# Performance work log

Measured on AMD Instinct MI355X. Metric: run time of the kernel, lower is better.

Reference implementation:

```python
import jax, jax.numpy as jnp
import numpy as np

N_NODES = 100000
N_EDGES = 300000
IN_DIM = 256
NUM_CLASSES = 64


def setup_inputs() -> dict:
    key = jax.random.key(0)
    k1, k2, k3, k4 = jax.random.split(key, 4)
    x = jax.random.normal(k1, (N_NODES, IN_DIM), dtype=jnp.float32)
    src = jax.random.randint(k2, (N_EDGES,), 0, N_NODES, dtype=jnp.int64 if jax.config.jax_enable_x64 else jnp.int32)
    dst = jax.random.randint(k3, (N_EDGES,), 0, N_NODES, dtype=jnp.int64 if jax.config.jax_enable_x64 else jnp.int32)
    W = jax.random.normal(k4, (2 * IN_DIM, IN_DIM * 0 + NUM_CLASSES), dtype=jnp.float32) * (1.0 / np.sqrt(2 * IN_DIM))
    b = jnp.zeros((NUM_CLASSES,), dtype=jnp.float32)
    return {"x": x, "src": src, "dst": dst, "W": W, "b": b}


def reference(x, src, dst, W, b):
    # score_e = Linear(concat(x[src_e], x[dst_e]))
    # Split W into src/dst halves to avoid materializing the [E, 2*d] concat.
    d = x.shape[-1]
    W_src, W_dst = W[:d], W[d:]            # each [d, C]
    score = x[src] @ W_src + x[dst] @ W_dst + b  # [E, C]
    return score
```

## Files before the change

### kernel.cpp

```cpp
#include <hip/hip_runtime.h>

#define N_NODES 100000
#define N_EDGES 300000
#define IN_DIM 256
#define NUM_CLASSES 64
#define YDIM 128

typedef __attribute__((ext_vector_type(8))) short short8;
typedef __attribute__((ext_vector_type(4))) float f32x4;

static __device__ __forceinline__ unsigned short f2bf(float f) {
    union { float f; unsigned u; } v; v.f = f;
    unsigned r = v.u + 0x7FFFu + ((v.u >> 16) & 1u);
    return (unsigned short)(r >> 16);
}

__global__ __launch_bounds__(256) void node_gemm_mfma(const float* __restrict__ x,
                                                      const float* __restrict__ W,
                                                      float* __restrict__ Y) {
    __shared__ unsigned short Wlds[YDIM * IN_DIM];

    const int t    = threadIdx.x;
    const int lane = t & 63;
    const int wv   = t >> 6;
    const int g    = lane >> 4;
    const int ln   = lane & 15;

    {
        const int n     = t & 127;
        const int kbase = (t >> 7) * 128;
        for (int i = 0; i < 64; ++i) {
            const int k = kbase + i * 2;
            float f0, f1;
            if (n < NUM_CLASSES) {
                f0 = W[(size_t)k * NUM_CLASSES + n];
                f1 = W[(size_t)(k + 1) * NUM_CLASSES + n];
            } else {
                f0 = W[(size_t)(IN_DIM + k) * NUM_CLASSES + (n - NUM_CLASSES)];
                f1 = W[(size_t)(IN_DIM + k + 1) * NUM_CLASSES + (n - NUM_CLASSES)];
            }
            const unsigned v = (unsigned)f2bf(f0) | ((unsigned)f2bf(f1) << 16);
            int addr = n * 512 + k * 2;
            addr ^= (n & 7) << 4;
            *reinterpret_cast<unsigned*>(reinterpret_cast<char*>(Wlds) + addr) = v;
        }
    }
    __syncthreads();

    const int rowbase = blockIdx.x * 128 + wv * 32;

    f32x4 acc[2][8];
#pragma unroll
    for (int s = 0; s < 2; ++s)
#pragma unroll
        for (int nt = 0; nt < 8; ++nt)
            acc[s][nt] = (f32x4){0.f, 0.f, 0.f, 0.f};

    const int r0 = min(rowbase + ln,      N_NODES - 1);
    const int r1 = min(rowbase + 16 + ln, N_NODES - 1);
    const float* xr0 = x + (size_t)r0 * IN_DIM;
    const float* xr1 = x + (size_t)r1 * IN_DIM;

#pragma unroll 2
    for (int kk = 0; kk < 8; ++kk) {
        const int k0 = kk * 32 + g * 8;

        short8 a0, a1;
        {
            const float4 u = *reinterpret_cast<const float4*>(xr0 + k0);
            const float4 w_ = *reinterpret_cast<const float4*>(xr0 + k0 + 4);
            a0[0] = (short)f2bf(u.x);  a0[1] = (short)f2bf(u.y);
            a0[2] = (short)f2bf(u.z);  a0[3] = (short)f2bf(u.w);
            a0[4] = (short)f2bf(w_.x); a0[5] = (short)f2bf(w_.y);
            a0[6] = (short)f2bf(w_.z); a0[7] = (short)f2bf(w_.w);
        }
        {
            const float4 u = *reinterpret_cast<const float4*>(xr1 + k0);
            const float4 w_ = *reinterpret_cast<const float4*>(xr1 + k0 + 4);
            a1[0] = (short)f2bf(u.x);  a1[1] = (short)f2bf(u.y);
            a1[2] = (short)f2bf(u.z);  a1[3] = (short)f2bf(u.w);
            a1[4] = (short)f2bf(w_.x); a1[5] = (short)f2bf(w_.y);
            a1[6] = (short)f2bf(w_.z); a1[7] = (short)f2bf(w_.w);
        }

        short8 bfr[8];
#pragma unroll
        for (int nt = 0; nt < 8; ++nt) {
            const int row = nt * 16 + ln;
            int addr = row * 512 + k0 * 2;
            addr ^= (row & 7) << 4;
            bfr[nt] = *reinterpret_cast<const short8*>(
                reinterpret_cast<const char*>(Wlds) + addr);
        }

#pragma unroll
        for (int nt = 0; nt < 8; ++nt) {
            acc[0][nt] = __builtin_amdgcn_mfma_f32_16x16x32_bf16(a0, bfr[nt], acc[0][nt], 0, 0, 0);
            acc[1][nt] = __builtin_amdgcn_mfma_f32_16x16x32_bf16(a1, bfr[nt], acc[1][nt], 0, 0, 0);
        }
    }

#pragma unroll
    for (int s = 0; s < 2; ++s) {
#pragma unroll
        for (int r = 0; r < 4; ++r) {
            const int grow = rowbase + s * 16 + 4 * g + r;
            if (grow < N_NODES) {
                float* yrow = Y + (size_t)grow * YDIM;
#pragma unroll
                for (int nt = 0; nt < 8; ++nt)
                    yrow[nt * 16 + ln] = acc[s][nt][r];
            }
        }
    }
}

__global__ __launch_bounds__(256) void edge_combine(const int* __restrict__ src,
                                                    const int* __restrict__ dst,
                                                    const float* __restrict__ Y,
                                                    const float* __restrict__ b,
                                                    float* __restrict__ out) {
    int t = blockIdx.x * 256 + threadIdx.x;
    int e = t >> 4;
    int part = t & 15;
    if (e >= N_EDGES) return;

    int s = src[e];
    int d = dst[e];

    float4 ys = *reinterpret_cast<const float4*>(Y + (size_t)s * YDIM + part * 4);
    float4 yd = *reinterpret_cast<const float4*>(Y + (size_t)d * YDIM + 64 + part * 4);
    float4 bv = *reinterpret_cast<const float4*>(b + part * 4);

    float4 o;
    o.x = ys.x + yd.x + bv.x;
    o.y = ys.y + yd.y + bv.y;
    o.z = ys.z + yd.z + bv.z;
    o.w = ys.w + yd.w + bv.w;

    *reinterpret_cast<float4*>(out + (size_t)e * NUM_CLASSES + part * 4) = o;
}

extern "C" void kernel_launch(void* const* d_in, const int* in_sizes, int n_in,
                              void* d_out, int out_size, void* d_ws, size_t ws_size,
                              hipStream_t stream) {
    const float* x   = (const float*)d_in[0];
    const int*   src = (const int*)d_in[1];
    const int*   dst = (const int*)d_in[2];
    const float* W   = (const float*)d_in[3];
    const float* b   = (const float*)d_in[4];
    float* out = (float*)d_out;

    float* Y = (float*)d_ws;

    int blocksA = (N_NODES + 127) / 128;
    node_gemm_mfma<<<blocksA, 256, 0, stream>>>(x, W, Y);

    int blocksB = (N_EDGES * 16 + 255) / 256;
    edge_combine<<<blocksB, 256, 0, stream>>>(src, dst, Y, b, out);
}
```

Before: 231.2 us.

## Stream x tiles via async LDS double-buffer and store projected Y as bf16

The node GEMM now stages x into LDS with global_load_lds in a double-buffered 32-step pipeline. Each block covers 256 rows as four 64-row tiles, which amortises the W conversion across more rows. The intermediate Y table is written in bf16 instead of fp32, halving the gather traffic in the edge kernel, which now handles 8 columns per thread. This adds a __syncthreads per step and an extra bf16 rounding of Y, which reduces accuracy and halves the grid size of the first kernel.

```diff
diff --git a/kernel.cpp b/kernel.cpp
--- a/kernel.cpp
+++ b/kernel.cpp
@@ -14,11 +14,19 @@
     unsigned r = v.u + 0x7FFFu + ((v.u >> 16) & 1u);
     return (unsigned short)(r >> 16);
 }
+static __device__ __forceinline__ float bf2f(unsigned short u) {
+    union { unsigned u; float f; } v; v.u = ((unsigned)u) << 16;
+    return v.f;
+}
+
+typedef __attribute__((address_space(3))) unsigned char lds_byte;
+typedef const __attribute__((address_space(1))) unsigned char glb_byte;
 
 __global__ __launch_bounds__(256) void node_gemm_mfma(const float* __restrict__ x,
                                                       const float* __restrict__ W,
-                                                      float* __restrict__ Y) {
+                                                      unsigned short* __restrict__ Yb) {
     __shared__ unsigned short Wlds[YDIM * IN_DIM];
+    __shared__ float xb[2][2048];
 
     const int t    = threadIdx.x;
     const int lane = t & 63;
@@ -26,9 +34,31 @@
     const int g    = lane >> 4;
     const int ln   = lane & 15;
 
+    const int r0 = t >> 3;
+    const int p  = t & 7;
+    const int c0 = (p ^ (r0 & 7)) * 4;
+    const int blockbase = blockIdx.x * 256;
+
+    auto stage = [&](int s, int buf) {
+        const int tile = s >> 3, q = s & 7;
+        const int tb = blockbase + tile * 64;
+        int gr0 = tb + r0;      if (gr0 > N_NODES - 1) gr0 = N_NODES - 1;
+        int gr1 = tb + r0 + 32; if (gr1 > N_NODES - 1) gr1 = N_NODES - 1;
+        const float* src0 = x + (size_t)gr0 * IN_DIM + q * 32 + c0;
+        const float* src1 = x + (size_t)gr1 * IN_DIM + q * 32 + c0;
+        float* dst0 = &xb[buf][(r0 * 8 + p) * 4];
+        float* dst1 = &xb[buf][((r0 + 32) * 8 + p) * 4];
+        __builtin_amdgcn_global_load_lds((glb_byte*)src0, (lds_byte*)dst0, 16, 0, 0);
+        __builtin_amdgcn_global_load_lds((glb_byte*)src1, (lds_byte*)dst1, 16, 0, 0);
+    };
+
+    stage(0, 0);
+
     {
         const int n     = t & 127;
         const int kbase = (t >> 7) * 128;
+        const unsigned swz = (unsigned)((n & 7) << 4);
+#pragma unroll 4
         for (int i = 0; i < 64; ++i) {
             const int k = kbase + i * 2;
             float f0, f1;
@@ -40,105 +70,95 @@
                 f1 = W[(size_t)(IN_DIM + k + 1) * NUM_CLASSES + (n - NUM_CLASSES)];
             }
             const unsigned v = (unsigned)f2bf(f0) | ((unsigned)f2bf(f1) << 16);
-            int addr = n * 512 + k * 2;
-            addr ^= (n & 7) << 4;
+            const unsigned addr = (unsigned)(n * 512 + k * 2) ^ swz;
             *reinterpret_cast<unsigned*>(reinterpret_cast<char*>(Wlds) + addr) = v;
         }
     }
+
     __syncthreads();
 
-    const int rowbase = blockIdx.x * 128 + wv * 32;
+    f32x4 acc[8];
+#pragma unroll
+    for (int nt = 0; nt < 8; ++nt) acc[nt] = (f32x4){0.f, 0.f, 0.f, 0.f};
 
-    f32x4 acc[2][8];
-#pragma unroll
-    for (int s = 0; s < 2; ++s)
-#pragma unroll
-        for (int nt = 0; nt < 8; ++nt)
-            acc[s][nt] = (f32x4){0.f, 0.f, 0.f, 0.f};
-
-    const int r0 = min(rowbase + ln,      N_NODES - 1);
-    const int r1 = min(rowbase + 16 + ln, N_NODES - 1);
-    const float* xr0 = x + (size_t)r0 * IN_DIM;
-    const float* xr1 = x + (size_t)r1 * IN_DIM;
+    const int myrow = wv * 16 + ln;
+    const int a_ci0 = myrow * 8 + ((2 * g)     ^ (myrow & 7));
+    const int a_ci1 = myrow * 8 + ((2 * g + 1) ^ (myrow & 7));
 
 #pragma unroll 2
-    for (int kk = 0; kk < 8; ++kk) {
-        const int k0 = kk * 32 + g * 8;
+    for (int s = 0; s < 32; ++s) {
+        const int buf = s & 1;
+        if (s < 31) stage(s + 1, buf ^ 1);
 
-        short8 a0, a1;
-        {
-            const float4 u = *reinterpret_cast<const float4*>(xr0 + k0);
-            const float4 w_ = *reinterpret_cast<const float4*>(xr0 + k0 + 4);
-            a0[0] = (short)f2bf(u.x);  a0[1] = (short)f2bf(u.y);
-            a0[2] = (short)f2bf(u.z);  a0[3] = (short)f2bf(u.w);
-            a0[4] = (short)f2bf(w_.x); a0[5] = (short)f2bf(w_.y);
-            a0[6] = (short)f2bf(w_.z); a0[7] = (short)f2bf(w_.w);
-        }
-        {
-            const float4 u = *reinterpret_cast<const float4*>(xr1 + k0);
-            const float4 w_ = *reinterpret_cast<const float4*>(xr1 + k0 + 4);
-            a1[0] = (short)f2bf(u.x);  a1[1] = (short)f2bf(u.y);
-            a1[2] = (short)f2bf(u.z);  a1[3] = (short)f2bf(u.w);
-            a1[4] = (short)f2bf(w_.x); a1[5] = (short)f2bf(w_.y);
-            a1[6] = (short)f2bf(w_.z); a1[7] = (short)f2bf(w_.w);
+        const float4 af0 = *reinterpret_cast<const float4*>(&xb[buf][a_ci0 * 4]);
+        const float4 af1 = *reinterpret_cast<const float4*>(&xb[buf][a_ci1 * 4]);
+        short8 a;
+        a[0] = (short)f2bf(af0.x); a[1] = (short)f2bf(af0.y);
+        a[2] = (short)f2bf(af0.z); a[3] = (short)f2bf(af0.w);
+        a[4] = (short)f2bf(af1.x); a[5] = (short)f2bf(af1.y);
+        a[6] = (short)f2bf(af1.z); a[7] = (short)f2bf(af1.w);
+
+        const int q = s & 7;
+        const int kbyte = (q * 32 + g * 8) * 2;
+#pragma unroll
+        for (int nt = 0; nt < 8; ++nt) {
+            const int n = nt * 16 + ln;
+            const unsigned addr = (unsigned)(n * 512 + kbyte) ^ (unsigned)((n & 7) << 4);
+            const short8 bfr = *reinterpret_cast<const short8*>(
+                reinterpret_cast<const char*>(Wlds) + addr);
+            acc[nt] = __builtin_amdgcn_mfma_f32_16x16x32_bf16(a, bfr, acc[nt], 0, 0, 0);
         }
 
-        short8 bfr[8];
+        if (q == 7) {
+            const int rb = blockbase + (s >> 3) * 64 + wv * 16 + 4 * g;
 #pragma unroll
-        for (int nt = 0; nt < 8; ++nt) {
-            const int row = nt * 16 + ln;
-            int addr = row * 512 + k0 * 2;
-            addr ^= (row & 7) << 4;
-            bfr[nt] = *reinterpret_cast<const short8*>(
-                reinterpret_cast<const char*>(Wlds) + addr);
+            for (int r = 0; r < 4; ++r) {
+                if (rb + r < N_NODES) {
+                    unsigned short* yrow = Yb + (size_t)(rb + r) * YDIM;
+#pragma unroll
+                    for (int nt = 0; nt < 8; ++nt)
+                        yrow[nt * 16 + ln] = f2bf(acc[nt][r]);
+                }
+            }
+#pragma unroll
+            for (int nt = 0; nt < 8; ++nt) acc[nt] = (f32x4){0.f, 0.f, 0.f, 0.f};
         }
 
-#pragma unroll
-        for (int nt = 0; nt < 8; ++nt) {
-            acc[0][nt] = __builtin_amdgcn_mfma_f32_16x16x32_bf16(a0, bfr[nt], acc[0][nt], 0, 0, 0);
-            acc[1][nt] = __builtin_amdgcn_mfma_f32_16x16x32_bf16(a1, bfr[nt], acc[1][nt], 0, 0, 0);
-        }
-    }
-
-#pragma unroll
-    for (int s = 0; s < 2; ++s) {
-#pragma unroll
-        for (int r = 0; r < 4; ++r) {
-            const int grow = rowbase + s * 16 + 4 * g + r;
-            if (grow < N_NODES) {
-                float* yrow = Y + (size_t)grow * YDIM;
-#pragma unroll
-                for (int nt = 0; nt < 8; ++nt)
-                    yrow[nt * 16 + ln] = acc[s][nt][r];
-            }
-        }
+        __syncthreads();
     }
 }
 
 __global__ __launch_bounds__(256) void edge_combine(const int* __restrict__ src,
                                                     const int* __restrict__ dst,
-                                                    const float* __restrict__ Y,
+                                                    const unsigned short* __restrict__ Yb,
                                                     const float* __restrict__ b,
                                                     float* __restrict__ out) {
-    int t = blockIdx.x * 256 + threadIdx.x;
-    int e = t >> 4;
-    int part = t & 15;
+    const int t = blockIdx.x * 256 + threadIdx.x;
+    const int e = t >> 3;
+    const int part = t & 7;
     if (e >= N_EDGES) return;
 
-    int s = src[e];
-    int d = dst[e];
+    const int s = src[e];
+    const int d = dst[e];
 
-    float4 ys = *reinterpret_cast<const float4*>(Y + (size_t)s * YDIM + part * 4);
-    float4 yd = *reinterpret_cast<const float4*>(Y + (size_t)d * YDIM + 64 + part * 4);
-    float4 bv = *reinterpret_cast<const float4*>(b + part * 4);
+    const short8 ys = *reinterpret_cast<const short8*>(Yb + (size_t)s * YDIM + part * 8);
+    const short8 yd = *reinterpret_cast<const short8*>(Yb + (size_t)d * YDIM + 64 + part * 8);
+    const float4 b0 = *reinterpret_cast<const float4*>(b + part * 8);
+    const float4 b1 = *reinterpret_cast<const float4*>(b + part * 8 + 4);
 
-    float4 o;
-    o.x = ys.x + yd.x + bv.x;
-    o.y = ys.y + yd.y + bv.y;
-    o.z = ys.z + yd.z + bv.z;
-    o.w = ys.w + yd.w + bv.w;
+    float4 o0, o1;
+    o0.x = bf2f((unsigned short)ys[0]) + bf2f((unsigned short)yd[0]) + b0.x;
+    o0.y = bf2f((unsigned short)ys[1]) + bf2f((unsigned short)yd[1]) + b0.y;
+    o0.z = bf2f((unsigned short)ys[2]) + bf2f((unsigned short)yd[2]) + b0.z;
+    o0.w = bf2f((unsigned short)ys[3]) + bf2f((unsigned short)yd[3]) + b0.w;
+    o1.x = bf2f((unsigned short)ys[4]) + bf2f((unsigned short)yd[4]) + b1.x;
+    o1.y = bf2f((unsigned short)ys[5]) + bf2f((unsigned short)yd[5]) + b1.y;
+    o1.z = bf2f((unsigned short)ys[6]) + bf2f((unsigned short)yd[6]) + b1.z;
+    o1.w = bf2f((unsigned short)ys[7]) + bf2f((unsigned short)yd[7]) + b1.w;
 
-    *reinterpret_cast<float4*>(out + (size_t)e * NUM_CLASSES + part * 4) = o;
+    float* op = out + (size_t)e * NUM_CLASSES + part * 8;
+    *reinterpret_cast<float4*>(op)     = o0;
+    *reinterpret_cast<float4*>(op + 4) = o1;
 }
 
 extern "C" void kernel_launch(void* const* d_in, const int* in_sizes, int n_in,
@@ -151,11 +171,11 @@
     const float* b   = (const float*)d_in[4];
     float* out = (float*)d_out;
 
-    float* Y = (float*)d_ws;
+    unsigned short* Yb = (unsigned short*)d_ws;
 
-    int blocksA = (N_NODES + 127) / 128;
-    node_gemm_mfma<<<blocksA, 256, 0, stream>>>(x, W, Y);
+    const int blocksA = (N_NODES + 255) / 256;
+    node_gemm_mfma<<<blocksA, 256, 0, stream>>>(x, W, Yb);
 
-    int blocksB = (N_EDGES * 16 + 255) / 256;
-    edge_combine<<<blocksB, 256, 0, stream>>>(src, dst, Y, b, out);
+    const int blocksB = (N_EDGES * 8 + 255) / 256;
+    edge_combine<<<blocksB, 256, 0, stream>>>(src, dst, Yb, b, out);
 }
```

Measured after the change: 214.5 us. -7.2%, faster.
